# Kernel optimization log

Hardware: AMD Instinct MI355X
Metric: run time of the kernel (lower is better)

## Reference

```python
import jax, jax.numpy as jnp
import numpy as np

D, M, N = 1024, 16, 16384
H = D // M  # head dim = 64
C = 10.0    # tanh logit clipping


def setup_inputs() -> dict:
    key = jax.random.key(0)
    kb, kq, km, k1, k2, k3, k4 = jax.random.split(key, 7)
    def xavier(k, shape):
        # torch xavier_uniform: fan_in = prod(shape[1:]), fan_out = shape[0]*prod(shape[2:])
        fan_in = int(np.prod(shape[1:]))
        fan_out = shape[0] * int(np.prod(shape[2:]))
        bound = float(np.sqrt(6.0 / (fan_in + fan_out)))
        return jax.random.uniform(k, shape, jnp.float32, -bound, bound)
    return {
        "b": jax.random.normal(kb, (N, D), jnp.float32),
        "q_s_bar": jax.random.normal(kq, (D,), jnp.float32),
        "mask": jax.random.randint(km, (N,), 0, 2).astype(bool),
        "W_k_bar": xavier(k1, (M, H, D)),
        "W_v_bar": xavier(k2, (M, H, D)),
        "W_k": xavier(k3, (D, D)),
        "W_q": xavier(k4, (D, D)),
    }


def reference(b, q_s_bar, mask, W_k_bar, W_v_bar, W_k, W_q):
    # k_bar, v_bar: (N, M, H)  == matmul(W, b.t()).permute(2,0,1)
    k_bar = jnp.einsum('mhd,nd->nmh', W_k_bar, b)
    v_bar = jnp.einsum('mhd,nd->nmh', W_v_bar, b)
    k = b @ W_k.T                      # (N, D) == matmul(W_k, b.t()).t()
    q = q_s_bar.reshape(M, H)          # (M, H)
    # c_bar: (N, M, M) == matmul(k_bar, q.T) / sqrt(h)
    c_bar = jnp.einsum('nmh,gh->nmg', k_bar, q) / np.float32(np.sqrt(H))
    scores = jnp.where(mask[:, None, None], c_bar, -jnp.inf)
    attn = jax.nn.softmax(scores, axis=0)          # softmax over N
    # (N,M,M) @ (N,M,H) batched -> (N,M,H); view(N,-1).sum(0) -> (D,)
    q_s = jnp.einsum('nmg,ngh->nmh', attn, v_bar).reshape(N, D).sum(0)
    c = (k @ (W_q @ q_s)) / np.float32(np.sqrt(D))  # (N,)
    c = C * jnp.tanh(c)
    return jnp.where(mask, c, -jnp.inf)
```

## Files before the change

kernel.cpp:

```cpp
#include <hip/hip_runtime.h>
#include <math.h>
#include <float.h>

#define NN 16384
#define DD 1024
#define MM 16
#define HH 64
#define MG 256

typedef __attribute__((ext_vector_type(8))) short bh8;
typedef __attribute__((ext_vector_type(4))) float f32x4;

__device__ inline float bf2f(unsigned short u) {
    union { unsigned int i; float f; } v;
    v.i = ((unsigned int)u) << 16;
    return v.f;
}

__device__ inline unsigned short f2bf(float f) {
    union { float f; unsigned int i; } v;
    v.f = f;
    unsigned int r = v.i + 0x7FFFu + ((v.i >> 16) & 1u);
    return (unsigned short)(r >> 16);
}

__device__ inline float ld1(const void* p, long i, int isf) {
    return isf ? ((const float*)p)[i] : bf2f(((const unsigned short*)p)[i]);
}

__device__ inline float4 ld4(const void* p, long i, int isf) {
    if (isf) return *(const float4*)((const float*)p + i);
    ushort4 u = *(const ushort4*)((const unsigned short*)p + i);
    return make_float4(bf2f(u.x), bf2f(u.y), bf2f(u.z), bf2f(u.w));
}

__device__ inline bool get_mask(const unsigned char* mp, int n, int flag) {
    return flag ? (mp[n] != 0) : (mp[4 * n] != 0);
}

__device__ inline void gl_lds16(const void* g, void* l) {
    __builtin_amdgcn_global_load_lds(
        (const __attribute__((address_space(1))) unsigned int*)g,
        (__attribute__((address_space(3))) unsigned int*)l, 16, 0, 0);
}

__global__ void detect(const unsigned char* __restrict__ mp,
                       const unsigned char* __restrict__ bb, int* flags,
                       float* __restrict__ u, float* __restrict__ l) {
    int i = blockIdx.x * 256 + threadIdx.x;
    if (i < DD) u[i] = 0.f;
    if (i < MG) l[i] = 0.f;
    int v1 = ((i & 3) != 0 && mp[i] != 0) ? 1 : 0;
    unsigned char c = bb[4 * i + 1];
    bool expish = (c == 0x00) || (c == 0x80) || (c >= 0x30 && c <= 0x47) ||
                  (c >= 0xB0 && c <= 0xC7);
    int v2 = expish ? 0 : 1;
    unsigned long long b1 = __ballot(v1);
    unsigned long long b2 = __ballot(v2);
    if ((threadIdx.x & 63) == 0) {
        if (b1) atomicOr(&flags[0], 1);
        if (b2) atomicOr(&flags[1], 1);
    }
}

__global__ __launch_bounds__(256) void prep(const void* __restrict__ bB,
                                            unsigned short* __restrict__ bbf,
                                            unsigned short* __restrict__ bT,
                                            const void* __restrict__ Wkb,
                                            const void* __restrict__ qsb,
                                            unsigned short* __restrict__ Abf,
                                            const int* __restrict__ flags) {
    __shared__ unsigned short tl[2][32 * 68];
    const int isf = flags[1];
    const int bid = blockIdx.x;
    const int t = threadIdx.x;

    if (bid < 512) {
        const int n0 = bid * 32;
        const int r = t >> 3, c8 = (t & 7) * 8;
        const int dT = t >> 2, ch = t & 3;
        const long gbase = (long)(n0 + r) * DD + c8;

        float cur[8], nxt[8];
        auto LOAD = [&](float* dst, int dt) {
            if (isf) {
                float4 v0 = *(const float4*)((const float*)bB + gbase + dt * 64);
                float4 v1 = *(const float4*)((const float*)bB + gbase + dt * 64 + 4);
                dst[0] = v0.x; dst[1] = v0.y; dst[2] = v0.z; dst[3] = v0.w;
                dst[4] = v1.x; dst[5] = v1.y; dst[6] = v1.z; dst[7] = v1.w;
            } else {
                bh8 v = *(const bh8*)((const unsigned short*)bB + gbase + dt * 64);
#pragma unroll
                for (int j = 0; j < 8; j++) dst[j] = bf2f((unsigned short)v[j]);
            }
        };

        LOAD(cur, 0);
#pragma unroll
        for (int dt = 0; dt < 16; dt++) {
            if (dt < 15) LOAD(nxt, dt + 1);
            bh8 o;
#pragma unroll
            for (int j = 0; j < 8; j++) o[j] = (short)f2bf(cur[j]);
            *(bh8*)&bbf[gbase + dt * 64] = o;
            unsigned short* row = &tl[dt & 1][r * 68 + c8];
            ushort4 lo, hi;
            lo.x = (unsigned short)o[0]; lo.y = (unsigned short)o[1];
            lo.z = (unsigned short)o[2]; lo.w = (unsigned short)o[3];
            hi.x = (unsigned short)o[4]; hi.y = (unsigned short)o[5];
            hi.z = (unsigned short)o[6]; hi.w = (unsigned short)o[7];
            *(ushort4*)row = lo;
            *(ushort4*)(row + 4) = hi;
            __syncthreads();
            bh8 y;
#pragma unroll
            for (int k = 0; k < 8; k++)
                y[k] = (short)tl[dt & 1][(ch * 8 + k) * 68 + dT];
            *(bh8*)&bT[(long)(dt * 64 + dT) * NN + n0 + ch * 8] = y;
#pragma unroll
            for (int j = 0; j < 8; j++) cur[j] = nxt[j];
        }
    } else {
        float* q = (float*)tl;
        int b2 = bid - 512;
        int m = b2 >> 2;
        int d = (b2 & 3) * 256 + t;
        for (int i = t; i < DD; i += 256) q[i] = ld1(qsb, i, isf);
        __syncthreads();
        float acc[MM];
#pragma unroll
        for (int g = 0; g < MM; g++) acc[g] = 0.f;
        for (int h = 0; h < HH; h++) {
            float wv = ld1(Wkb, (long)(m * HH + h) * DD + d, isf);
#pragma unroll
            for (int g = 0; g < MM; g++) acc[g] += wv * q[g * HH + h];
        }
#pragma unroll
        for (int g = 0; g < MM; g++)
            Abf[(long)(m * MM + g) * DD + d] = f2bf(acc[g] * 0.125f);
    }
}

__global__ __launch_bounds__(256) void gemm_b_mfma(
    const unsigned short* __restrict__ Abf, const unsigned short* __restrict__ bbf,
    const unsigned char* __restrict__ mp, const int* __restrict__ flags,
    unsigned short* __restrict__ Cb, float* __restrict__ l) {
    __shared__ __align__(16) unsigned short As[64 * 128];
    __shared__ __align__(16) unsigned short Bs[64 * 128];
    __shared__ float lsum[64];
    int i = blockIdx.x;
    int xcd = i & 7, j = i >> 3;
    int mb = j & 3;
    int nsl = xcd | ((j >> 2) << 3);
    int m0 = mb * 64, n0 = nsl * 64;
    int t = threadIdx.x;
    int lane = t & 63, w = t >> 6;
    int wm = w >> 1, wn = w & 1;
    int r = lane & 15, q = lane >> 4;
    f32x4 acc[2][2] = {};
    for (int k0 = 0; k0 < DD; k0 += 128) {
#pragma unroll
        for (int i2 = 0; i2 < 4; i2++) {
            int L = (i2 * 4 + w) * 64 + lane;
            int row = L >> 4, c = (L & 15) ^ (row & 7);
            gl_lds16(&Abf[(long)(m0 + row) * DD + k0 + c * 8], &As[(i2 * 4 + w) * 512]);
        }
#pragma unroll
        for (int i2 = 0; i2 < 4; i2++) {
            int L = (i2 * 4 + w) * 64 + lane;
            int row = L >> 4, c = (L & 15) ^ (row & 7);
            gl_lds16(&bbf[(long)(n0 + row) * DD + k0 + c * 8], &Bs[(i2 * 4 + w) * 512]);
        }
        __syncthreads();
#pragma unroll
        for (int h = 0; h < 4; h++) {
            bh8 af[2], bfr[2];
#pragma unroll
            for (int fi = 0; fi < 2; fi++) {
                int row = wm * 32 + fi * 16 + r;
                int ck = (h * 4 + q) ^ (row & 7);
                af[fi] = *(const bh8*)&As[row * 128 + ck * 8];
            }
#pragma unroll
            for (int fj = 0; fj < 2; fj++) {
                int row = wn * 32 + fj * 16 + r;
                int ck = (h * 4 + q) ^ (row & 7);
                bfr[fj] = *(const bh8*)&Bs[row * 128 + ck * 8];
            }
#pragma unroll
            for (int fi = 0; fi < 2; fi++)
#pragma unroll
                for (int fj = 0; fj < 2; fj++)
                    acc[fi][fj] = __builtin_amdgcn_mfma_f32_16x16x32_bf16(
                        af[fi], bfr[fj], acc[fi][fj], 0, 0, 0);
        }
        __syncthreads();
    }
    if (t < 64) lsum[t] = 0.f;
    __syncthreads();
    int mflag = flags[0];
    float pv[2][2][4];
#pragma unroll
    for (int fj = 0; fj < 2; fj++) {
        int gn = n0 + wn * 32 + fj * 16 + r;
        bool mk = get_mask(mp, gn, mflag);
#pragma unroll
        for (int fi = 0; fi < 2; fi++)
#pragma unroll
            for (int reg = 0; reg < 4; reg++) {
                float e = mk ? expf(acc[fi][fj][reg] - 8.0f) : 0.f;
                int gm = m0 + wm * 32 + fi * 16 + q * 4 + reg;
                Cb[(long)gm * NN + gn] = f2bf(e);
                pv[fi][fj][reg] = e;
            }
    }
#pragma unroll
    for (int fi = 0; fi < 2; fi++)
#pragma unroll
        for (int reg = 0; reg < 4; reg++)
            atomicAdd(&lsum[wm * 32 + fi * 16 + q * 4 + reg],
                      pv[fi][0][reg] + pv[fi][1][reg]);
    __syncthreads();
    if (t < 64) atomicAdd(&l[m0 + t], lsum[t]);
}

__global__ __launch_bounds__(256) void gemm_d_mfma(
    const unsigned short* __restrict__ Cb, const unsigned short* __restrict__ bT,
    unsigned short* __restrict__ Tpart) {
    __shared__ __align__(16) unsigned short As[64 * 128];
    __shared__ __align__(16) unsigned short Bs[64 * 128];
    int i = blockIdx.x;
    int xcd = i & 7, j = i >> 3;
    int z = xcd | ((j >> 6) << 3);
    int inner = j & 63;
    int mb = inner >> 4, db = inner & 15;
    int m0 = mb * 64, d0 = db * 64;
    long kbase = (long)z * 1024;
    unsigned short* Cg = Tpart + (long)z * (MG * DD);
    int t = threadIdx.x;
    int lane = t & 63, w = t >> 6;
    int wm = w >> 1, wn = w & 1;
    int r = lane & 15, q = lane >> 4;
    f32x4 acc[2][2] = {};
    for (int k0 = 0; k0 < 1024; k0 += 128) {
#pragma unroll
        for (int i2 = 0; i2 < 4; i2++) {
            int L = (i2 * 4 + w) * 64 + lane;
            int row = L >> 4, c = (L & 15) ^ (row & 7);
            gl_lds16(&Cb[(long)(m0 + row) * NN + kbase + k0 + c * 8], &As[(i2 * 4 + w) * 512]);
        }
#pragma unroll
        for (int i2 = 0; i2 < 4; i2++) {
            int L = (i2 * 4 + w) * 64 + lane;
            int row = L >> 4, c = (L & 15) ^ (row & 7);
            gl_lds16(&bT[(long)(d0 + row) * NN + kbase + k0 + c * 8], &Bs[(i2 * 4 + w) * 512]);
        }
        __syncthreads();
#pragma unroll
        for (int h = 0; h < 4; h++) {
            bh8 af[2], bfr[2];
#pragma unroll
            for (int fi = 0; fi < 2; fi++) {
                int row = wm * 32 + fi * 16 + r;
                int ck = (h * 4 + q) ^ (row & 7);
                af[fi] = *(const bh8*)&As[row * 128 + ck * 8];
            }
#pragma unroll
            for (int fj = 0; fj < 2; fj++) {
                int row = wn * 32 + fj * 16 + r;
                int ck = (h * 4 + q) ^ (row & 7);
                bfr[fj] = *(const bh8*)&Bs[row * 128 + ck * 8];
            }
#pragma unroll
            for (int fi = 0; fi < 2; fi++)
#pragma unroll
                for (int fj = 0; fj < 2; fj++)
                    acc[fi][fj] = __builtin_amdgcn_mfma_f32_16x16x32_bf16(
                        af[fi], bfr[fj], acc[fi][fj], 0, 0, 0);
        }
        __syncthreads();
    }
#pragma unroll
    for (int fi = 0; fi < 2; fi++)
#pragma unroll
        for (int fj = 0; fj < 2; fj++)
#pragma unroll
            for (int reg = 0; reg < 4; reg++) {
                int gm = m0 + wm * 32 + fi * 16 + q * 4 + reg;
                int gd = d0 + wn * 32 + fj * 16 + r;
                Cg[(long)gm * DD + gd] = f2bf(acc[fi][fj][reg]);
            }
}

__global__ void reduce_T(const unsigned short* __restrict__ Tpart,
                         const float* __restrict__ l, float* __restrict__ T) {
    long i = (long)(blockIdx.x * 256 + threadIdx.x) * 8;
    int row = (int)(i >> 10);
    float li = l[row];
    float inv = (li > 0.f) ? 1.0f / li : 0.f;
    float s[8] = {};
#pragma unroll
    for (int c = 0; c < 16; c++) {
        bh8 v = *(const bh8*)&Tpart[(long)c * (MG * DD) + i];
#pragma unroll
        for (int j = 0; j < 8; j++) s[j] += bf2f((unsigned short)v[j]);
    }
#pragma unroll
    for (int j = 0; j < 8; j++) s[j] *= inv;
    *(float4*)&T[i] = make_float4(s[0], s[1], s[2], s[3]);
    *(float4*)&T[i + 4] = make_float4(s[4], s[5], s[6], s[7]);
}

__global__ void fold_v(const void* __restrict__ Wvb, const float* __restrict__ T,
                       float* __restrict__ qs, const int* __restrict__ flags) {
    int isf = flags[1];
    int w = threadIdx.x >> 6, lane = threadIdx.x & 63;
    int o = blockIdx.x * 4 + w;
    int m = o >> 6, h = o & 63;
    float s = 0.f;
    for (int g = 0; g < MM; g++) {
        const float* Trow = T + (long)(m * MM + g) * DD;
        long wbase = (long)(g * HH + h) * DD;
#pragma unroll
        for (int k = 0; k < 4; k++) {
            int d = lane * 4 + k * 256;
            float4 tv = *(const float4*)&Trow[d];
            float4 wv = ld4(Wvb, wbase + d, isf);
            s += wv.x * tv.x + wv.y * tv.y + wv.z * tv.z + wv.w * tv.w;
        }
    }
    for (int off = 32; off; off >>= 1) s += __shfl_down(s, off, 64);
    if (lane == 0) qs[o] = s;
}

__global__ void matvec_rows(const void* __restrict__ W, const float* __restrict__ x,
                            float* __restrict__ y, const int* __restrict__ flags) {
    int isf = flags[1];
    int lane = threadIdx.x & 63;
    int r = blockIdx.x * 4 + (threadIdx.x >> 6);
    long base = (long)r * DD;
    float s = 0.f;
#pragma unroll
    for (int k = 0; k < 4; k++) {
        int j = lane * 4 + k * 256;
        float4 wv = ld4(W, base + j, isf);
        float4 xv = *(const float4*)&x[j];
        s += wv.x * xv.x + wv.y * xv.y + wv.z * xv.z + wv.w * xv.w;
    }
    for (int off = 32; off; off >>= 1) s += __shfl_down(s, off, 64);
    if (lane == 0) y[r] = s;
}

__global__ void matvec_col(const void* __restrict__ Wk, const float* __restrict__ w1,
                           float* __restrict__ u, const int* __restrict__ flags) {
    __shared__ float xs[16];
    int isf = flags[1];
    int d = blockIdx.x * 256 + threadIdx.x;
    int i0 = blockIdx.y * 16;
    if (threadIdx.x < 16) xs[threadIdx.x] = w1[i0 + threadIdx.x];
    __syncthreads();
    float s = 0.f;
#pragma unroll
    for (int ii = 0; ii < 16; ii++) s += ld1(Wk, (long)(i0 + ii) * DD + d, isf) * xs[ii];
    atomicAdd(&u[d], s);
}

__global__ void final_k(const unsigned short* __restrict__ bbf, const float* __restrict__ u,
                        const unsigned char* __restrict__ mp, const int* __restrict__ flags,
                        void* __restrict__ out) {
    int mflag = flags[0];
    int isf = flags[1];
    int n = blockIdx.x * 4 + (threadIdx.x >> 6);
    int lane = threadIdx.x & 63;
    const unsigned short* row = bbf + (long)n * DD;
    float s = 0.f;
#pragma unroll
    for (int k = 0; k < 4; k++) {
        int j = lane * 4 + k * 256;
        ushort4 v = *(const ushort4*)&row[j];
        float4 uu = *(const float4*)&u[j];
        s += bf2f(v.x) * uu.x + bf2f(v.y) * uu.y + bf2f(v.z) * uu.z + bf2f(v.w) * uu.w;
    }
    for (int off = 32; off; off >>= 1) s += __shfl_down(s, off, 64);
    if (lane == 0) {
        float c = 10.f * tanhf(s * (1.0f / 32.0f));
        bool mk = get_mask(mp, n, mflag);
        if (isf) {
            union { unsigned int i; float f; } vv;
            vv.i = mk ? (((unsigned int)f2bf(c)) << 16) : 0xFF7F0000u;
            ((float*)out)[n] = vv.f;
        } else {
            ((unsigned short*)out)[n] = mk ? f2bf(c) : (unsigned short)0xFF7F;
        }
    }
}

extern "C" void kernel_launch(void* const* d_in, const int* in_sizes, int n_in,
                              void* d_out, int out_size, void* d_ws, size_t ws_size,
                              hipStream_t stream) {
    const void* b = d_in[0];
    const void* qsb = d_in[1];
    const unsigned char* mp = (const unsigned char*)d_in[2];
    const void* Wkb = d_in[3];
    const void* Wvb = d_in[4];
    const void* Wk = d_in[5];
    const void* Wq = d_in[6];

    char* ws = (char*)d_ws;
    unsigned short* bbf = (unsigned short*)(ws);
    unsigned short* bT = (unsigned short*)(ws + (32u << 20));
    unsigned short* Cb = (unsigned short*)(ws + (64u << 20));
    unsigned short* Tpart = (unsigned short*)(ws + (72u << 20));
    unsigned short* Abf = (unsigned short*)(ws + (88u << 20));
    float* T = (float*)(ws + (89u << 20));
    float* small = (float*)(ws + (90u << 20));
    float* qs = small;
    float* w1 = qs + 1024;
    float* u = w1 + 1024;
    float* l = u + 1024;
    int* flags = (int*)(l + 256);

    hipMemsetAsync(flags, 0, 2 * sizeof(int), stream);

    detect<<<64, 256, 0, stream>>>(mp, (const unsigned char*)b, flags, u, l);
    prep<<<576, 256, 0, stream>>>(b, bbf, bT, Wkb, qsb, Abf, flags);
    gemm_b_mfma<<<1024, 256, 0, stream>>>(Abf, bbf, mp, flags, Cb, l);
    gemm_d_mfma<<<1024, 256, 0, stream>>>(Cb, bT, Tpart);
    reduce_T<<<128, 256, 0, stream>>>(Tpart, l, T);
    fold_v<<<256, 256, 0, stream>>>(Wvb, T, qs, flags);
    matvec_rows<<<256, 256, 0, stream>>>(Wq, qs, w1, flags);
    matvec_col<<<dim3(4, 64), 256, 0, stream>>>(Wk, w1, u, flags);
    final_k<<<4096, 256, 0, stream>>>(bbf, u, mp, flags, d_out);
}
```

Before: 219.3 us.

## Retile prep transpose into 64x64 blocks and skip bf16 copy for bf16 inputs

The prep kernel now handles 64x64 tiles of b across 4096 blocks instead of 32-row strips. When the input is already bf16, it stages each tile through LDS with an XOR swizzle and writes only the transpose. The downstream GEMM and the final kernel then read the original input directly instead of a converted copy. This avoids a redundant bf16 copy of b in that case and gives more parallelism, at the cost of extra branching and a larger grid.

```diff
diff --git a/kernel.cpp b/kernel.cpp
--- a/kernel.cpp
+++ b/kernel.cpp
@@ -70,59 +70,62 @@
                                             const void* __restrict__ qsb,
                                             unsigned short* __restrict__ Abf,
                                             const int* __restrict__ flags) {
-    __shared__ unsigned short tl[2][32 * 68];
+    __shared__ __align__(16) unsigned short tl[64 * 64];
     const int isf = flags[1];
     const int bid = blockIdx.x;
     const int t = threadIdx.x;
 
-    if (bid < 512) {
-        const int n0 = bid * 32;
-        const int r = t >> 3, c8 = (t & 7) * 8;
-        const int dT = t >> 2, ch = t & 3;
-        const long gbase = (long)(n0 + r) * DD + c8;
-
-        float cur[8], nxt[8];
-        auto LOAD = [&](float* dst, int dt) {
-            if (isf) {
-                float4 v0 = *(const float4*)((const float*)bB + gbase + dt * 64);
-                float4 v1 = *(const float4*)((const float*)bB + gbase + dt * 64 + 4);
-                dst[0] = v0.x; dst[1] = v0.y; dst[2] = v0.z; dst[3] = v0.w;
-                dst[4] = v1.x; dst[5] = v1.y; dst[6] = v1.z; dst[7] = v1.w;
-            } else {
-                bh8 v = *(const bh8*)((const unsigned short*)bB + gbase + dt * 64);
-#pragma unroll
-                for (int j = 0; j < 8; j++) dst[j] = bf2f((unsigned short)v[j]);
-            }
-        };
-
-        LOAD(cur, 0);
-#pragma unroll
-        for (int dt = 0; dt < 16; dt++) {
-            if (dt < 15) LOAD(nxt, dt + 1);
-            bh8 o;
-#pragma unroll
-            for (int j = 0; j < 8; j++) o[j] = (short)f2bf(cur[j]);
-            *(bh8*)&bbf[gbase + dt * 64] = o;
-            unsigned short* row = &tl[dt & 1][r * 68 + c8];
-            ushort4 lo, hi;
-            lo.x = (unsigned short)o[0]; lo.y = (unsigned short)o[1];
-            lo.z = (unsigned short)o[2]; lo.w = (unsigned short)o[3];
-            hi.x = (unsigned short)o[4]; hi.y = (unsigned short)o[5];
-            hi.z = (unsigned short)o[6]; hi.w = (unsigned short)o[7];
-            *(ushort4*)row = lo;
-            *(ushort4*)(row + 4) = hi;
+    if (bid < 4096) {
+        const int n0 = (bid >> 4) * 64, d0 = (bid & 15) * 64;
+        const int dg = t & 15, ng = t >> 4;
+        if (!isf) {
+            const unsigned short* bs = (const unsigned short*)bB;
+            const int lane = t & 63, w = t >> 6;
+#pragma unroll
+            for (int i2 = 0; i2 < 2; i2++) {
+                int nl = i2 * 32 + w * 8 + (lane >> 3);
+                int sc = (lane & 7) ^ (nl & 7);
+                gl_lds16(&bs[(long)(n0 + nl) * DD + d0 + sc * 8],
+                         &tl[(i2 * 32 + w * 8) * 64]);
+            }
             __syncthreads();
-            bh8 y;
-#pragma unroll
-            for (int k = 0; k < 8; k++)
-                y[k] = (short)tl[dt & 1][(ch * 8 + k) * 68 + dT];
-            *(bh8*)&bT[(long)(dt * 64 + dT) * NN + n0 + ch * 8] = y;
-#pragma unroll
-            for (int j = 0; j < 8; j++) cur[j] = nxt[j];
+            ushort4 v[4];
+#pragma unroll
+            for (int k = 0; k < 4; k++) {
+                int nl = ng * 4 + k;
+                int byteoff = nl * 128 + ((((dg >> 1) ^ (nl & 7)) << 4)) + (dg & 1) * 8;
+                v[k] = *(const ushort4*)((const char*)tl + byteoff);
+            }
+#pragma unroll
+            for (int j = 0; j < 4; j++) {
+                ushort4 o;
+                o.x = (&v[0].x)[j]; o.y = (&v[1].x)[j];
+                o.z = (&v[2].x)[j]; o.w = (&v[3].x)[j];
+                *(ushort4*)&bT[(long)(d0 + dg * 4 + j) * NN + n0 + ng * 4] = o;
+            }
+        } else {
+            const float* bf = (const float*)bB;
+            ushort4 v[4];
+#pragma unroll
+            for (int k = 0; k < 4; k++) {
+                int nl = ng * 4 + k;
+                float4 f = *(const float4*)&bf[(long)(n0 + nl) * DD + d0 + dg * 4];
+                ushort4 o;
+                o.x = f2bf(f.x); o.y = f2bf(f.y); o.z = f2bf(f.z); o.w = f2bf(f.w);
+                v[k] = o;
+                *(ushort4*)&bbf[(long)(n0 + nl) * DD + d0 + dg * 4] = o;
+            }
+#pragma unroll
+            for (int j = 0; j < 4; j++) {
+                ushort4 o;
+                o.x = (&v[0].x)[j]; o.y = (&v[1].x)[j];
+                o.z = (&v[2].x)[j]; o.w = (&v[3].x)[j];
+                *(ushort4*)&bT[(long)(d0 + dg * 4 + j) * NN + n0 + ng * 4] = o;
+            }
         }
     } else {
         float* q = (float*)tl;
-        int b2 = bid - 512;
+        int b2 = bid - 4096;
         int m = b2 >> 2;
         int d = (b2 & 3) * 256 + t;
         for (int i = t; i < DD; i += 256) q[i] = ld1(qsb, i, isf);
@@ -142,12 +145,14 @@
 }
 
 __global__ __launch_bounds__(256) void gemm_b_mfma(
-    const unsigned short* __restrict__ Abf, const unsigned short* __restrict__ bbf,
+    const unsigned short* __restrict__ Abf, const void* __restrict__ bB,
+    const unsigned short* __restrict__ bbf,
     const unsigned char* __restrict__ mp, const int* __restrict__ flags,
     unsigned short* __restrict__ Cb, float* __restrict__ l) {
     __shared__ __align__(16) unsigned short As[64 * 128];
     __shared__ __align__(16) unsigned short Bs[64 * 128];
     __shared__ float lsum[64];
+    const unsigned short* Bsrc = flags[1] ? bbf : (const unsigned short*)bB;
     int i = blockIdx.x;
     int xcd = i & 7, j = i >> 3;
     int mb = j & 3;
@@ -169,7 +174,7 @@
         for (int i2 = 0; i2 < 4; i2++) {
             int L = (i2 * 4 + w) * 64 + lane;
             int row = L >> 4, c = (L & 15) ^ (row & 7);
-            gl_lds16(&bbf[(long)(n0 + row) * DD + k0 + c * 8], &Bs[(i2 * 4 + w) * 512]);
+            gl_lds16(&Bsrc[(long)(n0 + row) * DD + k0 + c * 8], &Bs[(i2 * 4 + w) * 512]);
         }
         __syncthreads();
 #pragma unroll
@@ -365,14 +370,17 @@
     atomicAdd(&u[d], s);
 }
 
-__global__ void final_k(const unsigned short* __restrict__ bbf, const float* __restrict__ u,
+__global__ void final_k(const void* __restrict__ bB,
+                        const unsigned short* __restrict__ bbf,
+                        const float* __restrict__ u,
                         const unsigned char* __restrict__ mp, const int* __restrict__ flags,
                         void* __restrict__ out) {
     int mflag = flags[0];
     int isf = flags[1];
+    const unsigned short* bbase = isf ? bbf : (const unsigned short*)bB;
     int n = blockIdx.x * 4 + (threadIdx.x >> 6);
     int lane = threadIdx.x & 63;
-    const unsigned short* row = bbf + (long)n * DD;
+    const unsigned short* row = bbase + (long)n * DD;
     float s = 0.f;
 #pragma unroll
     for (int k = 0; k < 4; k++) {
@@ -423,12 +431,12 @@
     hipMemsetAsync(flags, 0, 2 * sizeof(int), stream);
 
     detect<<<64, 256, 0, stream>>>(mp, (const unsigned char*)b, flags, u, l);
-    prep<<<576, 256, 0, stream>>>(b, bbf, bT, Wkb, qsb, Abf, flags);
-    gemm_b_mfma<<<1024, 256, 0, stream>>>(Abf, bbf, mp, flags, Cb, l);
+    prep<<<4160, 256, 0, stream>>>(b, bbf, bT, Wkb, qsb, Abf, flags);
+    gemm_b_mfma<<<1024, 256, 0, stream>>>(Abf, b, bbf, mp, flags, Cb, l);
     gemm_d_mfma<<<1024, 256, 0, stream>>>(Cb, bT, Tpart);
     reduce_T<<<128, 256, 0, stream>>>(Tpart, l, T);
     fold_v<<<256, 256, 0, stream>>>(Wvb, T, qs, flags);
     matvec_rows<<<256, 256, 0, stream>>>(Wq, qs, w1, flags);
     matvec_col<<<dim3(4, 64), 256, 0, stream>>>(Wk, w1, u, flags);
-    final_k<<<4096, 256, 0, stream>>>(bbf, u, mp, flags, d_out);
-}
+    final_k<<<4096, 256, 0, stream>>>(b, bbf, u, mp, flags, d_out);
+}
```

New measurement: 224.9 us. +2.5%, slower.
